# Optimization experiments

Measured on AMD Instinct MI355X. Metric: run time of the kernel, lower is better.

## Reference

```python
import jax, jax.numpy as jnp
import numpy as np

B, C, T = 8, 512, 8192
NQ, CBS, CBD = 9, 1024, 8
EPS = 1e-12  # F.normalize eps


def setup_inputs() -> dict:
    key = jax.random.key(0)
    ks = jax.random.split(key, 12)
    n = lambda i, shape, s: jax.random.normal(ks[i], shape, jnp.float32) * s
    return {
        "z": n(0, (B, C, T), 1.0),
        "down_w": n(1, (2, C, C, 2), 0.02),   # [layer, out, in, k] (torch Conv1d layout)
        "down_b": n(2, (2, C), 0.01),
        "up_w": n(3, (2, C, C, 2), 0.02),     # [layer, in, out, k] (torch ConvTranspose1d layout)
        "up_b": n(4, (2, C), 0.01),
        "in_v": n(5, (NQ, CBD, C), 0.05),     # weight_norm direction of in_proj 1x1 conv
        "in_g": 1.0 + n(6, (NQ, CBD), 0.02),  # weight_norm magnitude
        "in_b": n(7, (NQ, CBD), 0.01),
        "out_v": n(8, (NQ, C, CBD), 0.05),
        "out_g": 1.0 + n(9, (NQ, C), 0.02),
        "out_b": n(10, (NQ, C), 0.01),
        "codebooks": n(11, (NQ, CBS, CBD), 1.0),
    }


def _wn(g, v):
    # weight_norm (dim=0): per-output-row rescale
    return g[:, None] * v / jnp.linalg.norm(v, axis=1, keepdims=True)


def _l2norm(x):
    return x / jnp.maximum(jnp.linalg.norm(x, axis=-1, keepdims=True), EPS)


def _forward(z, down_w, down_b, up_w, up_b, in_v, in_g, in_b, out_v, out_g, out_b, codebooks):
    # --- downsample: two Conv1d(k=2, s=2) ---
    x = z
    for l in range(2):
        b, c, t = x.shape
        xr = x.reshape(b, c, t // 2, 2)
        x = jnp.einsum('bitk,oik->bot', xr, down_w[l]) + down_b[l][None, :, None]

    residual = x
    z_q = jnp.zeros_like(x)
    commit_loss = jnp.float32(0.0)
    cb_loss = jnp.float32(0.0)
    codes = []
    for i in range(NQ):
        # in_proj 1x1 conv (weight-normed)
        w_in = _wn(in_g[i], in_v[i])                 # [CBD, C]
        z_e = jnp.einsum('bdt,cd->bct', residual, w_in) + in_b[i][None, :, None]  # [B, CBD, T']
        # decode_latents: L2-normalize + squared-euclid via matmul + argmax
        bt = z_e.shape[0] * z_e.shape[2]
        enc = z_e.transpose(0, 2, 1).reshape(bt, CBD)
        enc_n = _l2norm(enc)
        cbk = codebooks[i]
        cb_n = _l2norm(cbk)
        dist = ((enc_n ** 2).sum(1, keepdims=True)
                - 2.0 * enc_n @ cb_n.T
                + (cb_n ** 2).sum(1)[None, :])        # [B*T', CBS]
        idx = jnp.argmax(-dist, axis=1).reshape(z_e.shape[0], -1)  # [B, T']
        z_q_i = cbk[idx].transpose(0, 2, 1)           # [B, CBD, T'] (un-normalized codebook rows)
        # losses (eval: mask all-true -> per-batch mean over (1,2) then batch mean == global mean)
        commit_loss = commit_loss + ((z_e - jax.lax.stop_gradient(z_q_i)) ** 2).mean()
        cb_loss = cb_loss + ((z_q_i - jax.lax.stop_gradient(z_e)) ** 2).mean()
        # straight-through + out_proj 1x1 conv (weight-normed)
        z_st = z_e + jax.lax.stop_gradient(z_q_i - z_e)
        w_out = _wn(out_g[i], out_v[i])               # [C, CBD]
        z_q_out = jnp.einsum('bct,dc->bdt', z_st, w_out) + out_b[i][None, :, None]
        z_q = z_q + z_q_out
        residual = residual - z_q_out
        codes.append(idx)
    codes = jnp.stack(codes, axis=1)                  # [B, NQ, T']

    x = z_q
    for l in range(2):
        b, c, t = x.shape
        x = jnp.einsum('bit,iok->botk', x, up_w[l]).reshape(b, C, t * 2) + up_b[l][None, :, None]
    return x, codes, commit_loss, cb_loss


def reference(z, down_w, down_b, up_w, up_b, in_v, in_g, in_b, out_v, out_g, out_b, codebooks):
    return _forward(z, down_w, down_b, up_w, up_b, in_v, in_g, in_b, out_v, out_g, out_b, codebooks)
```

## Files before the change

### kernel.cpp

```cpp
#include <hip/hip_runtime.h>
#include <math.h>


using u16 = unsigned short;
typedef __attribute__((ext_vector_type(8))) short bf16x8;
typedef __attribute__((ext_vector_type(8))) u16 su16x8;
typedef __attribute__((ext_vector_type(4))) float f32x4;

constexpr int NQ = 9, CBS = 1024, CBD = 8;
constexpr int TQ = 2048;
constexpr int NTOK = 16384;
constexpr int APS = 1048576;
#define EPSN 1e-12f

constexpr size_t OFF_X2    = 0;
constexpr size_t OFF_Q     = 9568256;
constexpr size_t OFF_WD    = 10878976;
constexpr size_t OFF_WDP   = 11927552;
constexpr size_t OFF_WEFF  = 13500416;
constexpr size_t OFF_WX    = 14548992;
constexpr size_t OFF_WINN  = 14712832;
constexpr size_t OFF_WOUTS = 14749696;
constexpr size_t OFF_CBS   = 14790656;
constexpr size_t OFF_PT    = 14809088;
constexpr size_t OFF_BEFF  = 14811428;
constexpr size_t OFF_BSUM  = 14811500;
constexpr size_t OFF_BD    = 14812012;
constexpr size_t OFF_BUP   = 14812524;
constexpr size_t OFF_LOSS  = 14813548;

__global__ __launch_bounds__(256) void prep_all1(const float* __restrict__ in_v,
                                                 const float* __restrict__ in_g,
                                                 const float* __restrict__ out_v,
                                                 const float* __restrict__ out_g,
                                                 const float* __restrict__ out_b,
                                                 const float* __restrict__ codebooks,
                                                 const float* __restrict__ down_w,
                                                 const float* __restrict__ down_b,
                                                 const float* __restrict__ up_w,
                                                 const float* __restrict__ up_b,
                                                 float* __restrict__ ws) {
  int bid = blockIdx.x, tid = threadIdx.x;
  if (bid < 206) {
    int wid4 = tid >> 6, lane = tid & 63;
    if (bid < 18) {
      int wid = bid * 4 + wid4;
      if (wid < 72) {
        const float* v = in_v + (size_t)wid * 512;
        float ss = 0.f;
        for (int c = lane; c < 512; c += 64) ss += v[c] * v[c];
        #pragma unroll
        for (int o = 32; o; o >>= 1) ss += __shfl_xor(ss, o);
        float sc = in_g[wid] / sqrtf(ss);
        float* dst = ws + OFF_WINN + (size_t)wid * 512;
        for (int c = lane; c < 512; c += 64) dst[c] = v[c] * sc;
      }
    } else if (bid < 36) {
      int r = (bid - 18) * 256 + tid;
      if (r < 4608) {
        int i = r >> 9, c = r & 511;
        const float* v = out_v + (size_t)r * 8;
        float ss = 0.f;
        #pragma unroll
        for (int d = 0; d < 8; d++) ss += v[d] * v[d];
        float sc = out_g[r] / sqrtf(ss);
        float* dst = ws + OFF_WOUTS + (size_t)c * 80 + i * 8;
        #pragma unroll
        for (int d = 0; d < 8; d++) dst[d] = v[d] * sc;
      }
    } else if (bid < 72) {
      int r = (bid - 36) * 256 + tid;
      if (r < 9216) {
        int i = r >> 10, j = r & 1023;
        const float* v = codebooks + (size_t)r * 8;
        float ss = 0.f;
        #pragma unroll
        for (int d = 0; d < 8; d++) ss += v[d] * v[d];
        float nm = fmaxf(sqrtf(ss), EPSN);
        float nsq = 0.f;
        #pragma unroll
        for (int d = 0; d < 8; d++) { float cn = v[d] / nm; nsq += cn * cn; }
        ws[OFF_CBS + ((size_t)i * 2 + 0) * 1024 + j] = 2.0f / nm;
        ws[OFF_CBS + ((size_t)i * 2 + 1) * 1024 + j] = nsq;
      }
    } else if (bid < 74) {
      int c = (bid - 72) * 256 + tid;
      if (c < 512) {
        float s = 0.f;
        #pragma unroll
        for (int j = 0; j < 9; j++) s += out_b[j * 512 + c];
        ws[OFF_BSUM + c] = s;
        ws[OFF_WOUTS + (size_t)c * 80 + 72] = s;
        #pragma unroll
        for (int d = 73; d < 80; d++) ws[OFF_WOUTS + (size_t)c * 80 + d] = 0.f;
      }
    } else if (bid < 202) {
      int o = (bid - 74) * 4 + wid4;
      float s = 0.f;
      for (int m = lane; m < 512; m += 64) {
        float w0 = down_w[524288 + (size_t)o * 1024 + m * 2];
        float w1 = down_w[524288 + (size_t)o * 1024 + m * 2 + 1];
        s += (w0 + w1) * down_b[m];
      }
      #pragma unroll
      for (int off = 32; off; off >>= 1) s += __shfl_xor(s, off);
      if (lane == 0) ws[OFF_BD + o] = s + down_b[512 + o];
    } else {
      int gw = (bid - 202) * 256 + tid;
      int c = gw >> 1, j2 = gw & 1;
      float s = 0.f;
      for (int m = 0; m < 512; m++)
        s += up_w[524288 + (size_t)m * 1024 + c * 2 + j2] * up_b[m];
      ws[OFF_BUP + gw] = s + up_b[512 + c];
    }
    return;
  }
  __shared__ float As[32][68];
  __shared__ float Bs[32][68];
  const int bid2 = bid - 206;
  const int tx = tid & 15, ty = tid >> 4;
  const int b0 = (bid2 & 7) * 64, a0 = ((bid2 >> 3) & 7) * 64;
  const int zz = bid2 >> 6;
  const int which = zz >> 2, j = zz & 3;
  const int jh = j >> 1, jl = j & 1;
  const float* src = which ? up_w : down_w;
  float acc[4][4];
  #pragma unroll
  for (int i = 0; i < 4; i++)
    #pragma unroll
    for (int k = 0; k < 4; k++) acc[i][k] = 0.f;

  for (int k0 = 0; k0 < 512; k0 += 32) {
    #pragma unroll
    for (int rep = 0; rep < 8; rep++) {
      int f = tid + rep * 256;
      int aa = f >> 5, mm = f & 31;
      size_t ai = which ? (524288 + (size_t)(k0 + mm) * 1024 + (a0 + aa) * 2 + jl)
                        : (524288 + (size_t)(a0 + aa) * 1024 + (k0 + mm) * 2 + jh);
      As[mm][aa] = src[ai];
      int mm2 = f >> 6, bb = f & 63;
      size_t bi = which ? ((size_t)(b0 + bb) * 1024 + (k0 + mm2) * 2 + jh)
                        : ((size_t)(k0 + mm2) * 1024 + (b0 + bb) * 2 + jl);
      Bs[mm2][bb] = src[bi];
    }
    __syncthreads();
    #pragma unroll
    for (int kk = 0; kk < 32; kk++) {
      float av[4], bv[4];
      #pragma unroll
      for (int i = 0; i < 4; i++) av[i] = As[kk][ty * 4 + i];
      #pragma unroll
      for (int i = 0; i < 4; i++) bv[i] = Bs[kk][tx * 4 + i];
      #pragma unroll
      for (int i = 0; i < 4; i++)
        #pragma unroll
        for (int k = 0; k < 4; k++) acc[i][k] = fmaf(av[i], bv[k], acc[i][k]);
    }
    __syncthreads();
  }
  float* wd = ws + OFF_WD;
  float* weff = ws + OFF_WEFF;
  #pragma unroll
  for (int i = 0; i < 4; i++) {
    int a = a0 + ty * 4 + i;
    #pragma unroll
    for (int k = 0; k < 4; k++) {
      int b = b0 + tx * 4 + k;
      if (which) weff[((size_t)a * 4 + j) * 512 + b] = acc[i][k];
      else       wd[(size_t)a * 2048 + b * 4 + j] = acc[i][k];
    }
  }
}

__global__ __launch_bounds__(256) void prep_all2(const float* __restrict__ in_b,
                                                 const float* __restrict__ out_b,
                                                 float* __restrict__ ws) {
  const int tid = threadIdx.x;
  if (blockIdx.x < 594) {
    int gw = blockIdx.x * 4 + (tid >> 6), lane = tid & 63;
    const float* WinN = ws + OFF_WINN;
    const float* WoutS = ws + OFF_WOUTS;
    if (gw < 2304) {
      int tri = gw >> 6, dd = gw & 63;
      int ip = 1;
      while (tri >= ip * (ip + 1) / 2) ip++;
      int i = tri - ip * (ip - 1) / 2;
      int d = dd >> 3, dp = dd & 7;
      const float* a = WinN + (size_t)(ip * 8 + d) * 512;
      float s = 0.f;
      for (int c = lane; c < 512; c += 64) s += a[c] * WoutS[(size_t)c * 80 + i * 8 + dp];
      #pragma unroll
      for (int o = 32; o; o >>= 1) s += __shfl_xor(s, o);
      if (lane == 0) ws[OFF_PT + (size_t)tri * 65 + dd] = s;
    } else if (gw < 2376) {
      int r = gw - 2304;
      int i = r >> 3;
      const float* a = WinN + (size_t)r * 512;
      float s = 0.f;
      for (int c = lane; c < 512; c += 64) {
        float ob = 0.f;
        for (int j = 0; j < i; j++) ob += out_b[j * 512 + c];
        s += a[c] * ob;
      }
      #pragma unroll
      for (int o = 32; o; o >>= 1) s += __shfl_xor(s, o);
      if (lane == 0) ws[OFF_BEFF + r] = in_b[r] - s;
    }
    return;
  }
  const int bid2 = blockIdx.x - 594;
  if (bid2 < 4096) {
    int idx = bid2 * 256 + tid;
    const float* wd = ws + OFF_WD;
    u16* wdp = (u16*)(ws + OFF_WDP);
    float v = wd[idx];
    unsigned u = __float_as_uint(v);
    wdp[idx] = (u16)(u >> 16);
    float r = v - __uint_as_float(u & 0xFFFF0000u);
    unsigned ur = __float_as_uint(r);
    wdp[APS + idx] = (u16)(ur >> 16);
    float r2 = r - __uint_as_float(ur & 0xFFFF0000u);
    wdp[2 * APS + idx] = (u16)(__float_as_uint(r2) >> 16);
    return;
  }
  __shared__ float Wes[16][512];
  __shared__ float WSs[64][80];
  const float* weff = ws + OFF_WEFF;
  const float* wouts = ws + OFF_WOUTS;
  float* wx = ws + OFF_WX;
  const int m0 = (bid2 - 4096) * 16;
  #pragma unroll
  for (int rep = 0; rep < 32; rep++) {
    int f = tid + rep * 256;
    Wes[f >> 9][f & 511] = weff[(size_t)(m0 + (f >> 9)) * 512 + (f & 511)];
  }
  const int rowq = tid >> 4, rq = tid & 15;
  float accs[5] = {0.f, 0.f, 0.f, 0.f, 0.f};
  for (int k0 = 0; k0 < 512; k0 += 64) {
    __syncthreads();
    #pragma unroll
    for (int rep = 0; rep < 20; rep++) {
      int f = tid + rep * 256;
      int kk = f / 80, col = f % 80;
      WSs[kk][col] = wouts[(size_t)(k0 + kk) * 80 + col];
    }
    __syncthreads();
    #pragma unroll 4
    for (int kk = 0; kk < 64; kk++) {
      float we = Wes[rowq][k0 + kk];
      #pragma unroll
      for (int s = 0; s < 5; s++) accs[s] = fmaf(we, WSs[kk][rq + 16 * s], accs[s]);
    }
  }
  #pragma unroll
  for (int s = 0; s < 5; s++) {
    int r = rq + 16 * s;
    if (r < 73) wx[(size_t)(m0 + rowq) * 80 + r] = accs[s];
  }
  if (tid < 112) {
    int row = tid / 7, col = 73 + tid % 7;
    wx[(size_t)(m0 + row) * 80 + col] = 0.f;
  }
}

__global__ __launch_bounds__(256) void gemm_down(const u16* __restrict__ Ap,
                                                 const float* __restrict__ z,
                                                 const float* __restrict__ bias,
                                                 float* __restrict__ Out) {
  constexpr int NS = 3, K = 2048;
  __shared__ u16 Bp[2][NS][128][32];
  const int tid = threadIdx.x;
  const int w = tid >> 6, l = tid & 63;
  const int g = l >> 4, li = l & 15;
  const int wr = w >> 1, wc = w & 1;
  const int n0 = blockIdx.x * 128, m0 = blockIdx.y * 128;
  const int nn = tid & 127, kw = tid >> 7;
  const int bb = n0 >> 11;
  const int tb = (n0 & 2047) + nn;

  f32x4 acc[4][4];
  #pragma unroll
  for (int a = 0; a < 4; a++)
    #pragma unroll
    for (int b = 0; b < 4; b++) acc[a][b] = (f32x4){0.f, 0.f, 0.f, 0.f};

  float pvA[16], pvB[16];

#define LOADB(PV, K0)                                                           \
  {                                                                             \
    int c0_ = ((K0) >> 2) + kw * 4;                                             \
    _Pragma("unroll")                                                           \
    for (int cc_ = 0; cc_ < 4; ++cc_)                                           \
      *(float4*)&PV[4 * cc_] =                                                  \
          *(const float4*)(z + ((size_t)(bb * 512 + c0_ + cc_) << 13) + 4 * tb);\
  }

  const int sw = (nn >> 1) & 3;
  const int c0 = ((2 * kw) ^ sw) << 3, c1 = ((2 * kw + 1) ^ sw) << 3;

#define STAGE(BUF, PV)                                                          \
  {                                                                             \
    su16x8 pa_[NS], pb_[NS];                                                    \
    _Pragma("unroll")                                                           \
    for (int j_ = 0; j_ < 8; ++j_) {                                            \
      {                                                                         \
        float v_ = PV[j_];                                                      \
        unsigned u_ = __float_as_uint(v_);                                      \
        pa_[0][j_] = (u16)(u_ >> 16);                                           \
        float r_ = v_ - __uint_as_float(u_ & 0xFFFF0000u);                      \
        unsigned ur_ = __float_as_uint(r_);                                     \
        pa_[1][j_] = (u16)(ur_ >> 16);                                          \
        float r2_ = r_ - __uint_as_float(ur_ & 0xFFFF0000u);                    \
        pa_[2][j_] = (u16)(__float_as_uint(r2_) >> 16);                         \
      }                                                                         \
      {                                                                         \
        float v_ = PV[8 + j_];                                                  \
        unsigned u_ = __float_as_uint(v_);                                      \
        pb_[0][j_] = (u16)(u_ >> 16);                                           \
        float r_ = v_ - __uint_as_float(u_ & 0xFFFF0000u);                      \
        unsigned ur_ = __float_as_uint(r_);                                     \
        pb_[1][j_] = (u16)(ur_ >> 16);                                          \
        float r2_ = r_ - __uint_as_float(ur_ & 0xFFFF0000u);                    \
        pb_[2][j_] = (u16)(__float_as_uint(r2_) >> 16);                         \
      }                                                                         \
    }                                                                           \
    _Pragma("unroll")                                                           \
    for (int p_ = 0; p_ < NS; ++p_) {                                           \
      *(su16x8*)&Bp[BUF][p_][nn][c0] = pa_[p_];                                 \
      *(su16x8*)&Bp[BUF][p_][nn][c1] = pb_[p_];                                 \
    }                                                                           \
  }

#define COMPUTE(BUF, K0)                                                        \
  {                                                                             \
    bf16x8 bfr_[4][NS];                                                         \
    _Pragma("unroll")                                                           \
    for (int fn_ = 0; fn_ < 4; ++fn_) {                                         \
      int row_ = wc * 64 + fn_ * 16 + li;                                       \
      int cs_ = ((g ^ ((row_ >> 1) & 3)) << 3);                                 \
      _Pragma("unroll")                                                         \
      for (int q_ = 0; q_ < NS; ++q_)                                           \
        bfr_[fn_][q_] = *(const bf16x8*)&Bp[BUF][q_][row_][cs_];                \
    }                                                                           \
    const u16* arow_ = Ap + (size_t)(m0 + wr * 64 + li) * K + (K0) + g * 8;     \
    _Pragma("unroll")                                                           \
    for (int fm_ = 0; fm_ < 4; ++fm_) {                                         \
      bf16x8 afr_[NS];                                                          \
      _Pragma("unroll")                                                         \
      for (int p_ = 0; p_ < NS; ++p_)                                           \
        afr_[p_] = *(const bf16x8*)(arow_ + (size_t)p_ * APS + (size_t)fm_ * 16 * K); \
      _Pragma("unroll")                                                         \
      for (int fn_ = 0; fn_ < 4; ++fn_) {                                       \
        f32x4 a_ = acc[fm_][fn_];                                               \
        a_ = __builtin_amdgcn_mfma_f32_16x16x32_bf16(afr_[2], bfr_[fn_][0], a_, 0, 0, 0); \
        a_ = __builtin_amdgcn_mfma_f32_16x16x32_bf16(afr_[1], bfr_[fn_][1], a_, 0, 0, 0); \
        a_ = __builtin_amdgcn_mfma_f32_16x16x32_bf16(afr_[0], bfr_[fn_][2], a_, 0, 0, 0); \
        a_ = __builtin_amdgcn_mfma_f32_16x16x32_bf16(afr_[1], bfr_[fn_][0], a_, 0, 0, 0); \
        a_ = __builtin_amdgcn_mfma_f32_16x16x32_bf16(afr_[0], bfr_[fn_][1], a_, 0, 0, 0); \
        a_ = __builtin_amdgcn_mfma_f32_16x16x32_bf16(afr_[0], bfr_[fn_][0], a_, 0, 0, 0); \
        acc[fm_][fn_] = a_;                                                     \
      }                                                                         \
    }                                                                           \
  }

  LOADB(pvA, 0)
  LOADB(pvB, 32)
  STAGE(0, pvA)
  LOADB(pvA, 64)
  __syncthreads();

  for (int k0 = 0; k0 < K; k0 += 64) {
    STAGE(1, pvB)
    if (k0 + 96 < K) { LOADB(pvB, k0 + 96) }
    COMPUTE(0, k0)
    __syncthreads();
    if (k0 + 64 < K) { STAGE(0, pvA) }
    if (k0 + 128 < K) { LOADB(pvA, k0 + 128) }
    COMPUTE(1, k0 + 32)
    __syncthreads();
  }
#undef LOADB
#undef STAGE
#undef COMPUTE

  const int mb = m0 + wr * 64 + g * 4;
  const int nb = n0 + wc * 64 + li;
  #pragma unroll
  for (int fn = 0; fn < 4; ++fn) {
    int n = nb + fn * 16;
    int b = n >> 11, t = n & 2047;
    #pragma unroll
    for (int fm = 0; fm < 4; ++fm)
      #pragma unroll
      for (int r = 0; r < 4; ++r) {
        int o = mb + fm * 16 + r;
        Out[((size_t)((b << 9) + o)) * 2048 + t] = acc[fm][fn][r] + bias[o];
      }
  }
}

__global__ __launch_bounds__(256) void rvq_kernel(const float* __restrict__ codebooks,
                                                  const float* __restrict__ x2,
                                                  const float* __restrict__ winn,
                                                  const float* __restrict__ cbsW,
                                                  const float* __restrict__ ptW,
                                                  const float* __restrict__ beffW,
                                                  float* __restrict__ Qout,
                                                  float* __restrict__ codesOut,
                                                  float* __restrict__ lossPart) {
  __shared__ float cbv[8][1024];
  __shared__ float cbs2[2][1024];
  __shared__ float est[16][72];
  __shared__ float lred[4];
  int tid = threadIdx.x, wid = tid >> 6, lane = tid & 63;
  int nb0 = blockIdx.x * 16;

  for (int idx = tid; idx < 1152; idx += 256) {
    int m = idx >> 4, tokl = idx & 15;
    int n = nb0 + tokl;
    int b = n >> 11, t = n & 2047;
    const float* xcol = x2 + ((size_t)b * 512) * 2048 + t;
    const float* wrow = winn + (size_t)m * 512;
    float acc = 0.f;
    for (int k = 0; k < 512; ++k)
      acc = fmaf(wrow[k], xcol[(size_t)k * 2048], acc);
    est[tokl][m] = acc + beffW[m];
  }
  float lossLocal = 0.f;

  for (int i = 0; i < NQ; i++) {
    __syncthreads();
    const float* cbg = codebooks + (size_t)i * CBS * CBD;
    for (int lin = tid; lin < 2048; lin += 256) {
      int j = lin >> 1, half = (lin & 1) << 2;
      float4 v = *(const float4*)(cbg + (size_t)j * 8 + half);
      cbv[half + 0][j] = v.x; cbv[half + 1][j] = v.y;
      cbv[half + 2][j] = v.z; cbv[half + 3][j] = v.w;
    }
    for (int lin = tid; lin < 1024; lin += 256) {
      cbs2[0][lin] = cbsW[((size_t)i * 2 + 0) * 1024 + lin];
      cbs2[1][lin] = cbsW[((size_t)i * 2 + 1) * 1024 + lin];
    }
    __syncthreads();

    float ze[4][8], en[4][8];
    #pragma unroll
    for (int w = 0; w < 4; w++) {
      int tokl = wid * 4 + w;
      float ss = 0.f;
      #pragma unroll
      for (int d = 0; d < 8; d++) { float v = est[tokl][i * 8 + d]; ze[w][d] = v; ss += v * v; }
      float inv = 1.0f / fmaxf(sqrtf(ss), EPSN);
      #pragma unroll
      for (int d = 0; d < 8; d++) en[w][d] = ze[w][d] * inv;
    }
    float best[4]; int bidx[4];
    #pragma unroll
    for (int w = 0; w < 4; w++) { best[w] = -INFINITY; bidx[w] = 0; }
    #pragma unroll 4
    for (int r = 0; r < 16; r++) {
      int j = lane + (r << 6);
      float c0 = cbv[0][j], c1 = cbv[1][j], c2 = cbv[2][j], c3 = cbv[3][j];
      float c4 = cbv[4][j], c5 = cbv[5][j], c6 = cbv[6][j], c7 = cbv[7][j];
      float ti = cbs2[0][j], ns = cbs2[1][j];
      #pragma unroll
      for (int w = 0; w < 4; w++) {
        float dt = en[w][0] * c0;
        dt = fmaf(en[w][1], c1, dt); dt = fmaf(en[w][2], c2, dt);
        dt = fmaf(en[w][3], c3, dt); dt = fmaf(en[w][4], c4, dt);
        dt = fmaf(en[w][5], c5, dt); dt = fmaf(en[w][6], c6, dt);
        dt = fmaf(en[w][7], c7, dt);
        float s = fmaf(dt, ti, -ns);
        if (s > best[w]) { best[w] = s; bidx[w] = j; }
      }
    }
    #pragma unroll
    for (int w = 0; w < 4; w++) {
      #pragma unroll
      for (int off = 32; off; off >>= 1) {
        float so = __shfl_xor(best[w], off);
        int jo = __shfl_xor(bidx[w], off);
        if (so > best[w] || (so == best[w] && jo < bidx[w])) { best[w] = so; bidx[w] = jo; }
      }
    }
    int d = lane & 7;
    #pragma unroll
    for (int w = 0; w < 4; w++) {
      int jstar = bidx[w];
      int tokl = wid * 4 + w;
      int n = nb0 + tokl;
      float qd = cbv[d][jstar];
      float diff = ze[w][d] - qd;
      float sq = diff * diff;
      sq += __shfl_xor(sq, 1); sq += __shfl_xor(sq, 2); sq += __shfl_xor(sq, 4);
      if (lane == 0) lossLocal += sq;
      if (lane < 8) Qout[(size_t)n * 80 + i * 8 + lane] = qd;
      if (lane == 0) codesOut[(size_t)((n >> 11) * NQ + i) * TQ + (n & (TQ - 1))] = (float)jstar;
      if (i < NQ - 1) {
        int f = lane >> 3, d2 = lane & 7;
        int ip = i + 1 + f;
        if (ip < NQ) {
          int tri = (ip * (ip - 1)) / 2 + i;
          const float* prow = ptW + (size_t)tri * 65 + d2 * 8;
          float s = 0.f;
          #pragma unroll
          for (int dp = 0; dp < 8; dp++) s = fmaf(prow[dp], cbv[dp][jstar], s);
          est[tokl][ip * 8 + d2] -= s;
        }
      }
    }
  }
  if (lane == 0) lred[wid] = lossLocal;
  __syncthreads();
  if (tid == 0) {
    float s = ((lred[0] + lred[1]) + lred[2]) + lred[3];
    lossPart[blockIdx.x] = s;
  }
}

__global__ __launch_bounds__(256) void xfin_loss(const float* __restrict__ wx,
                                                 const float* __restrict__ Q,
                                                 const float* __restrict__ bup,
                                                 const float* __restrict__ lossPart,
                                                 float* __restrict__ xout,
                                                 float* __restrict__ lossOut) {
  const int tid = threadIdx.x;
  if (blockIdx.x == 128) {
    if (blockIdx.y != 0) return;
    __shared__ float s[256];
    float v = 0.f;
    for (int r = 0; r < 4; r++) v += lossPart[tid + r * 256];
    s[tid] = v;
    __syncthreads();
    for (int w = 128; w; w >>= 1) {
      if (tid < w) s[tid] += s[tid + w];
      __syncthreads();
    }
    if (tid == 0) {
      float total = s[0] / 131072.0f;
      lossOut[0] = total;
      lossOut[1] = total;
    }
    return;
  }
  __shared__ float Wxs[128][80];
  __shared__ float Qs[128][80];
  const int n0 = blockIdx.x * 128, m0 = blockIdx.y * 128;
  #pragma unroll
  for (int rep = 0; rep < 10; rep++) {
    int f = tid + rep * 256;
    *(float4*)&Wxs[0][f * 4] = *(const float4*)(wx + (size_t)m0 * 80 + f * 4);
    *(float4*)&Qs[0][f * 4] = *(const float4*)(Q + (size_t)n0 * 80 + f * 4);
  }
  __syncthreads();

  const int txn = tid & 15, tym = tid >> 4;
  float acc[8][8];
  #pragma unroll
  for (int i = 0; i < 8; i++)
    #pragma unroll
    for (int j = 0; j < 8; j++) acc[i][j] = 0.f;

  #pragma unroll 2
  for (int r4 = 0; r4 < 18; r4++) {
    float4 wv[8], qv[8];
    #pragma unroll
    for (int i = 0; i < 8; i++) wv[i] = *(const float4*)&Wxs[tym * 8 + i][r4 * 4];
    #pragma unroll
    for (int j = 0; j < 8; j++) qv[j] = *(const float4*)&Qs[txn * 8 + j][r4 * 4];
    #pragma unroll
    for (int i = 0; i < 8; i++)
      #pragma unroll
      for (int j = 0; j < 8; j++) {
        acc[i][j] = fmaf(wv[i].x, qv[j].x, acc[i][j]);
        acc[i][j] = fmaf(wv[i].y, qv[j].y, acc[i][j]);
        acc[i][j] = fmaf(wv[i].z, qv[j].z, acc[i][j]);
        acc[i][j] = fmaf(wv[i].w, qv[j].w, acc[i][j]);
      }
  }

  float bxv[8];
  #pragma unroll
  for (int mi = 0; mi < 8; mi++) {
    int mp = m0 + tym * 8 + mi;
    bxv[mi] = Wxs[tym * 8 + mi][72] + bup[(mp >> 2) * 2 + (mp & 1)];
  }
  #pragma unroll
  for (int cg = 0; cg < 2; cg++) {
    int mp0 = m0 + tym * 8 + cg * 4;
    int c = mp0 >> 2;
    #pragma unroll
    for (int j = 0; j < 8; j++) {
      int n = n0 + txn * 8 + j;
      int b = n >> 11, t = n & 2047;
      float4 sv = make_float4(acc[cg * 4 + 0][j] + bxv[cg * 4 + 0],
                              acc[cg * 4 + 1][j] + bxv[cg * 4 + 1],
                              acc[cg * 4 + 2][j] + bxv[cg * 4 + 2],
                              acc[cg * 4 + 3][j] + bxv[cg * 4 + 3]);
      *(float4*)&xout[((size_t)((b << 9) + c)) * 8192 + 4 * t] = sv;
    }
  }
}

extern "C" void kernel_launch(void* const* d_in, const int* in_sizes, int n_in,
                              void* d_out, int out_size, void* d_ws, size_t ws_size,
                              hipStream_t stream) {
  const float* z      = (const float*)d_in[0];
  const float* down_w = (const float*)d_in[1];
  const float* down_b = (const float*)d_in[2];
  const float* up_w   = (const float*)d_in[3];
  const float* up_b   = (const float*)d_in[4];
  const float* in_v   = (const float*)d_in[5];
  const float* in_g   = (const float*)d_in[6];
  const float* in_b   = (const float*)d_in[7];
  const float* out_v  = (const float*)d_in[8];
  const float* out_g  = (const float*)d_in[9];
  const float* out_b  = (const float*)d_in[10];
  const float* codebooks = (const float*)d_in[11];
  float* ws = (float*)d_ws;
  float* xout = (float*)d_out;
  float* codesOut = xout + (size_t)8 * 512 * 8192;
  float* lossOut = codesOut + (size_t)8 * NQ * TQ;

  hipLaunchKernelGGL(prep_all1, dim3(718), dim3(256), 0, stream,
                     in_v, in_g, out_v, out_g, out_b, codebooks,
                     down_w, down_b, up_w, up_b, ws);
  hipLaunchKernelGGL(prep_all2, dim3(4818), dim3(256), 0, stream, in_b, out_b, ws);
  hipLaunchKernelGGL(gemm_down, dim3(128, 4), dim3(256), 0, stream,
                     (const u16*)(ws + OFF_WDP), z, ws + OFF_BD, ws + OFF_X2);
  hipLaunchKernelGGL(rvq_kernel, dim3(1024), dim3(256), 0, stream,
                     codebooks, ws + OFF_X2, ws + OFF_WINN,
                     ws + OFF_CBS, ws + OFF_PT, ws + OFF_BEFF,
                     ws + OFF_Q, codesOut, ws + OFF_LOSS);
  hipLaunchKernelGGL(xfin_loss, dim3(129, 16), dim3(256), 0, stream,
                     ws + OFF_WX, ws + OFF_Q, ws + OFF_BUP, ws + OFF_LOSS,
                     xout, lossOut);
}
```

Baseline: 915.0 us.

## Move initial in-projection of all quantizers into a separate tiled FP32 GEMM

The per-block naive dot-product loop inside rvq_kernel, which computed the 72 projections for 16 tokens with strided global reads over K=512, is replaced by a dedicated shared-memory tiled GEMM kernel. That kernel writes token-major projections to a new workspace region, and rvq_kernel now only loads them and adds the bias. This is meant to remove redundant, uncoalesced global loads of x2 and the weights from the RVQ kernel. The cost is one extra launch and an intermediate buffer round trip.

```diff
diff --git a/kernel.cpp b/kernel.cpp
--- a/kernel.cpp
+++ b/kernel.cpp
@@ -14,6 +14,7 @@
 #define EPSN 1e-12f
 
 constexpr size_t OFF_X2    = 0;
+constexpr size_t OFF_E0T   = 8388608;
 constexpr size_t OFF_Q     = 9568256;
 constexpr size_t OFF_WD    = 10878976;
 constexpr size_t OFF_WDP   = 11927552;
@@ -399,9 +400,66 @@
   }
 }
 
+__global__ __launch_bounds__(256) void gemm_e0f(const float* __restrict__ A,
+                                                const float* __restrict__ Bsrc,
+                                                float* __restrict__ e0t) {
+  constexpr int M = 72, K = 512, Tt = 2048;
+  __shared__ float As[16][132];
+  __shared__ float Bs[16][68];
+  int tid = threadIdx.x;
+  int tx = tid & 7, ty = tid >> 3;
+  int n0 = blockIdx.x * 64;
+  int b = n0 / Tt, t0 = n0 % Tt;
+  float acc[4][8];
+  #pragma unroll
+  for (int i = 0; i < 4; i++)
+    #pragma unroll
+    for (int j = 0; j < 8; j++) acc[i][j] = 0.f;
+
+  for (int k0 = 0; k0 < K; k0 += 16) {
+    #pragma unroll
+    for (int rep = 0; rep < 2; rep++) {
+      int f = tid + rep * 256;
+      int row = f >> 2, c4 = (f & 3) << 2;
+      int m = row, k = k0 + c4;
+      float4 v = make_float4(0.f, 0.f, 0.f, 0.f);
+      if (m < M) v = *(const float4*)(A + (size_t)m * K + k);
+      As[c4 + 0][row] = v.x; As[c4 + 1][row] = v.y;
+      As[c4 + 2][row] = v.z; As[c4 + 3][row] = v.w;
+    }
+    {
+      int kk = tid >> 4, n4 = (tid & 15) << 2;
+      float4 v = *(const float4*)(Bsrc + ((size_t)(b * K + k0 + kk)) * Tt + t0 + n4);
+      *(float4*)&Bs[kk][n4] = v;
+    }
+    __syncthreads();
+    #pragma unroll
+    for (int kk = 0; kk < 16; kk++) {
+      float a[4], bb[8];
+      #pragma unroll
+      for (int i = 0; i < 4; i++) a[i] = As[kk][ty * 4 + i];
+      *(float4*)&bb[0] = *(float4*)&Bs[kk][tx * 8];
+      *(float4*)&bb[4] = *(float4*)&Bs[kk][tx * 8 + 4];
+      #pragma unroll
+      for (int i = 0; i < 4; i++)
+        #pragma unroll
+        for (int j = 0; j < 8; j++) acc[i][j] = fmaf(a[i], bb[j], acc[i][j]);
+    }
+    __syncthreads();
+  }
+  #pragma unroll
+  for (int j = 0; j < 8; j++) {
+    int n = n0 + tx * 8 + j;
+    #pragma unroll
+    for (int i = 0; i < 4; i++) {
+      int m = ty * 4 + i;
+      if (m < M) e0t[(size_t)n * M + m] = acc[i][j];
+    }
+  }
+}
+
 __global__ __launch_bounds__(256) void rvq_kernel(const float* __restrict__ codebooks,
-                                                  const float* __restrict__ x2,
-                                                  const float* __restrict__ winn,
+                                                  const float* __restrict__ e0t,
                                                   const float* __restrict__ cbsW,
                                                   const float* __restrict__ ptW,
                                                   const float* __restrict__ beffW,
@@ -414,18 +472,8 @@
   __shared__ float lred[4];
   int tid = threadIdx.x, wid = tid >> 6, lane = tid & 63;
   int nb0 = blockIdx.x * 16;
-
-  for (int idx = tid; idx < 1152; idx += 256) {
-    int m = idx >> 4, tokl = idx & 15;
-    int n = nb0 + tokl;
-    int b = n >> 11, t = n & 2047;
-    const float* xcol = x2 + ((size_t)b * 512) * 2048 + t;
-    const float* wrow = winn + (size_t)m * 512;
-    float acc = 0.f;
-    for (int k = 0; k < 512; ++k)
-      acc = fmaf(wrow[k], xcol[(size_t)k * 2048], acc);
-    est[tokl][m] = acc + beffW[m];
-  }
+  for (int idx = tid; idx < 16 * 72; idx += 256)
+    est[idx / 72][idx % 72] = e0t[(size_t)nb0 * 72 + idx] + beffW[idx % 72];
   float lossLocal = 0.f;
 
   for (int i = 0; i < NQ; i++) {
@@ -628,9 +676,10 @@
   hipLaunchKernelGGL(prep_all2, dim3(4818), dim3(256), 0, stream, in_b, out_b, ws);
   hipLaunchKernelGGL(gemm_down, dim3(128, 4), dim3(256), 0, stream,
                      (const u16*)(ws + OFF_WDP), z, ws + OFF_BD, ws + OFF_X2);
+  hipLaunchKernelGGL(gemm_e0f, dim3(256), dim3(256), 0, stream,
+                     ws + OFF_WINN, ws + OFF_X2, ws + OFF_E0T);
   hipLaunchKernelGGL(rvq_kernel, dim3(1024), dim3(256), 0, stream,
-                     codebooks, ws + OFF_X2, ws + OFF_WINN,
-                     ws + OFF_CBS, ws + OFF_PT, ws + OFF_BEFF,
+                     codebooks, ws + OFF_E0T, ws + OFF_CBS, ws + OFF_PT, ws + OFF_BEFF,
                      ws + OFF_Q, codesOut, ws + OFF_LOSS);
   hipLaunchKernelGGL(xfin_loss, dim3(129, 16), dim3(256), 0, stream,
                      ws + OFF_WX, ws + OFF_Q, ws + OFF_BUP, ws + OFF_LOSS,
```

Result: faster. 798.1 us (-12.8%).
